# Optimization experiments

Hardware: AMD Instinct MI355X
Metric: run time of the kernel (lower is better)

Reference implementation:

```python
import jax, jax.numpy as jnp
import numpy as np

N_NODES = 100000
N_EDGES = 1600000
IN_FEAT = 64
OUT_FEAT = 64


def setup_inputs() -> dict:
    key = jax.random.key(0)
    k_feat, k_src, k_dst, k_tw, k_tb, k_pw, k_pb = jax.random.split(key, 7)
    bound = 1.0 / np.sqrt(IN_FEAT)
    return {
        "feat": jax.random.normal(k_feat, (N_NODES, IN_FEAT), dtype=jnp.float32),
        "src": jax.random.randint(k_src, (N_EDGES,), 0, N_NODES, dtype=jnp.int32),
        "dst": jax.random.randint(k_dst, (N_EDGES,), 0, N_NODES, dtype=jnp.int32),
        "theta_w": jax.random.uniform(k_tw, (OUT_FEAT, IN_FEAT), jnp.float32, -bound, bound),
        "theta_b": jax.random.uniform(k_tb, (OUT_FEAT,), jnp.float32, -bound, bound),
        "phi_w": jax.random.uniform(k_pw, (OUT_FEAT, IN_FEAT), jnp.float32, -bound, bound),
        "phi_b": jax.random.uniform(k_pb, (OUT_FEAT,), jnp.float32, -bound, bound),
    }


def reference(feat, src, dst, theta_w, theta_b, phi_w, phi_b):
    # Two dense projections: h_theta = theta(feat), h_phi = phi(feat)
    h_theta = feat @ theta_w.T + theta_b          # [N, out_feat]
    h_phi = feat @ phi_w.T + phi_b                # [N, out_feat]
    diff = h_phi - h_theta                        # dstdata['x']
    # u_add_v: per-edge message e = h_theta[src] + (h_phi - h_theta)[dst]
    e = h_theta[src] + diff[dst]                  # [E, out_feat]
    # fn.max('e', 'x'): segment max over destination nodes
    out = jax.ops.segment_max(e, dst, num_segments=N_NODES)  # [N, out_feat]
    # DGL fills zero-in-degree destinations with 0 (segment_max yields -inf)
    return jnp.where(jnp.isfinite(out), out, jnp.float32(0))
```

## Files before the change

### kernel.cpp

```cpp
#include <hip/hip_runtime.h>
#include <hip/hip_bf16.h>
#include <hip/hip_fp16.h>

#define F 64
#define BSH 7
#define NBMAX 1024
#define BPAD 16
#define CHUNK 4096
#define EPT 8
#define BCAP 4096
#define WPAD 72

typedef __bf16 bf16x8 __attribute__((ext_vector_type(8)));
typedef float  f32x4  __attribute__((ext_vector_type(4)));
typedef unsigned int uint4v __attribute__((ext_vector_type(4)));

__device__ inline unsigned pkmax(unsigned a, unsigned b) {
    unsigned d;
    asm volatile("v_pk_max_f16 %0, %1, %2" : "=v"(d) : "v"(a), "v"(b));
    return d;
}
__device__ inline uint4v pkmax4(uint4v a, uint4v b) {
    uint4v r;
    r.x = pkmax(a.x, b.x); r.y = pkmax(a.y, b.y);
    r.z = pkmax(a.z, b.z); r.w = pkmax(a.w, b.w);
    return r;
}
__device__ inline float half_lo(unsigned u) {
    union { unsigned short s; _Float16 h; } c; c.s = (unsigned short)(u & 0xFFFF);
    return (float)c.h;
}
__device__ inline float half_hi(unsigned u) {
    union { unsigned short s; _Float16 h; } c; c.s = (unsigned short)(u >> 16);
    return (float)c.h;
}
__device__ inline void casmax(unsigned* a, unsigned val) {
    unsigned old = *a;
    while (true) {
        unsigned nw = pkmax(old, val);
        if (nw == old) break;
        unsigned prev = atomicCAS(a, old, nw);
        if (prev == old) break;
        old = prev;
    }
}

union FusedSh {
    struct { __bf16 w2t[128 * WPAD]; float bias[128]; } p;
    struct {
        int cur[NBMAX]; int gb[NBMAX]; int lbeg[NBMAX];
        int fs[512];
        unsigned sw[CHUNK];
        unsigned short sb[CHUNK];
    } b;
};

__global__ __launch_bounds__(512) void fused_proj_bin(
    const float* __restrict__ feat,
    const float* __restrict__ theta_w, const float* __restrict__ theta_b,
    const float* __restrict__ phi_w,  const float* __restrict__ phi_b,
    _Float16* __restrict__ h16, _Float16* __restrict__ d16,
    const int* __restrict__ src, const int* __restrict__ dst,
    int* __restrict__ bcnt, unsigned* __restrict__ packed,
    int n_nodes, int n_edges, int nb, int bin_blocks, int proj_blocks)
{
    __shared__ FusedSh sh;
    const int t = threadIdx.x;

    if (blockIdx.x < bin_blocks) {
        const int base = blockIdx.x * CHUNK;
        const int cnt = min(CHUNK, n_edges - base);

        for (int i = t; i < NBMAX; i += 512) sh.b.cur[i] = 0;
        __syncthreads();

        unsigned w[EPT];
        int      bk[EPT];
        int      rk[EPT];
        const int k0 = t * EPT;

        if (k0 + EPT <= cnt) {
            #pragma unroll
            for (int j = 0; j < EPT; ++j) {
                int k = k0 + j;
                int s = src[base + k], d = dst[base + k];
                w[j]  = ((unsigned)(d & ((1 << BSH) - 1)) << 17) | (unsigned)s;
                int b = d >> BSH;
                bk[j] = b;
                rk[j] = atomicAdd(&sh.b.cur[b], 1);
            }
        } else {
            #pragma unroll
            for (int j = 0; j < EPT; ++j) {
                int k = k0 + j;
                bk[j] = -1;
                if (k < cnt) {
                    int s = src[base + k], d = dst[base + k];
                    w[j]  = ((unsigned)(d & ((1 << BSH) - 1)) << 17) | (unsigned)s;
                    int b = d >> BSH;
                    bk[j] = b;
                    rk[j] = atomicAdd(&sh.b.cur[b], 1);
                }
            }
        }
        __syncthreads();

        for (int i = t; i < nb; i += 512) {
            int c = sh.b.cur[i];
            sh.b.gb[i] = c ? atomicAdd(&bcnt[i * BPAD], c) : 0;
        }

        int c0 = sh.b.cur[2 * t];
        int c1 = sh.b.cur[2 * t + 1];
        int s2 = c0 + c1;
        sh.b.fs[t] = s2;
        __syncthreads();
        for (int off = 1; off < 512; off <<= 1) {
            int x = (t >= off) ? sh.b.fs[t - off] : 0;
            __syncthreads();
            sh.b.fs[t] += x;
            __syncthreads();
        }
        {
            int exc = sh.b.fs[t] - s2;
            sh.b.lbeg[2 * t]     = exc;
            sh.b.lbeg[2 * t + 1] = exc + c0;
        }
        __syncthreads();

        #pragma unroll
        for (int j = 0; j < EPT; ++j) {
            if (bk[j] >= 0) {
                int slot = sh.b.lbeg[bk[j]] + rk[j];
                sh.b.sw[slot] = w[j];
                sh.b.sb[slot] = (unsigned short)bk[j];
            }
        }
        __syncthreads();

        #pragma unroll
        for (int r = 0; r < EPT; ++r) {
            int p = r * 512 + t;
            if (p < cnt) {
                int b = sh.b.sb[p];
                int pos = sh.b.gb[b] + (p - sh.b.lbeg[b]);
                if (pos < BCAP) packed[(size_t)b * BCAP + pos] = sh.b.sw[p];
            }
        }
    } else {
        const int pb = blockIdx.x - bin_blocks;

        for (int i = t; i < 128 * 64; i += 512) {
            int n = i >> 6, k = i & 63;
            float v = (n < 64) ? theta_w[n * 64 + k]
                               : phi_w[(n - 64) * 64 + k] - theta_w[(n - 64) * 64 + k];
            sh.p.w2t[n * WPAD + k] = (__bf16)v;
        }
        if (t < 128) {
            int n = t;
            sh.p.bias[n] = (n < 64) ? theta_b[n] : (phi_b[n - 64] - theta_b[n - 64]);
        }
        __syncthreads();

        const int lane = t & 63;
        const int wv   = t >> 6;
        const int m    = lane & 15;
        const int q    = lane >> 4;
        const int nchunks = (n_nodes + 127) >> 7;

        for (int ch = pb; ch < nchunks; ch += proj_blocks) {
            const int rowbase = ch * 128 + wv * 16;
            int arow = rowbase + m;
            int rs = arow < n_nodes ? arow : 0;

            bf16x8 a0, a1;
            {
                const float* p0 = feat + (size_t)rs * 64 + q * 8;
                #pragma unroll
                for (int j = 0; j < 8; ++j) a0[j] = (__bf16)p0[j];
                #pragma unroll
                for (int j = 0; j < 8; ++j) a1[j] = (__bf16)p0[32 + j];
            }

            f32x4 acc[8];
            #pragma unroll
            for (int c = 0; c < 8; ++c) acc[c] = (f32x4){0.f, 0.f, 0.f, 0.f};

            #pragma unroll
            for (int c = 0; c < 8; ++c) {
                const __bf16* wp = &sh.p.w2t[(c * 16 + m) * WPAD + q * 8];
                bf16x8 b0 = *(const bf16x8*)wp;
                bf16x8 b1 = *(const bf16x8*)(wp + 32);
                acc[c] = __builtin_amdgcn_mfma_f32_16x16x32_bf16(a0, b0, acc[c], 0, 0, 0);
                acc[c] = __builtin_amdgcn_mfma_f32_16x16x32_bf16(a1, b1, acc[c], 0, 0, 0);
            }

            #pragma unroll
            for (int c = 0; c < 8; ++c) {
                float bb = sh.p.bias[c * 16 + m];
                #pragma unroll
                for (int r = 0; r < 4; ++r) {
                    int orow = rowbase + q * 4 + r;
                    if (orow < n_nodes) {
                        float v = acc[c][r] + bb;
                        if (c < 4)
                            h16[(size_t)orow * F + c * 16 + m] = (_Float16)v;
                        else
                            d16[(size_t)orow * F + (c - 4) * 16 + m] = (_Float16)v;
                    }
                }
            }
        }
    }
}

__global__ __launch_bounds__(256) void sort_reduce(
    const unsigned* __restrict__ packed, const int* __restrict__ bcnt,
    const _Float16* __restrict__ h16, const _Float16* __restrict__ d16,
    float* __restrict__ out, int n_nodes)
{
    __shared__ unsigned ew[BCAP];
    __shared__ unsigned mx[128 * 32];
    __shared__ int fcnt[128];
    __shared__ int fbg[129];
    __shared__ int fs[256];

    const int b = blockIdx.x, t = threadIdx.x;
    const int beg = b * BCAP;
    const int cnt = min(bcnt[b * BPAD], BCAP);
    const unsigned NEGI = 0xFC00FC00u;

    #pragma unroll
    for (int i = 0; i < 16; ++i) mx[i * 256 + t] = NEGI;
    if (t < 128) fcnt[t] = 0;
    __syncthreads();

    unsigned w[16];
    int      rk[16];
    #pragma unroll
    for (int j = 0; j < 16; ++j) {
        int k = j * 256 + t;
        rk[j] = -1;
        if (k < cnt) {
            unsigned wrd = packed[beg + k];
            w[j]  = wrd;
            rk[j] = atomicAdd(&fcnt[wrd >> 17], 1);
        }
    }
    __syncthreads();

    int v = (t < 128) ? fcnt[t] : 0;
    fs[t] = v;
    __syncthreads();
    for (int off = 1; off < 128; off <<= 1) {
        int x = (t >= off) ? fs[t - off] : 0;
        __syncthreads();
        fs[t] += x;
        __syncthreads();
    }
    if (t < 128) fbg[t] = fs[t] - v;
    if (t == 0)  fbg[128] = cnt;
    __syncthreads();

    #pragma unroll
    for (int j = 0; j < 16; ++j) {
        if (rk[j] >= 0) {
            unsigned wrd = w[j];
            ew[fbg[wrd >> 17] + rk[j]] = wrd & 0x1FFFFu;
        }
    }
    __syncthreads();

    const int g  = t >> 3;
    const int f8 = t & 7;
    {
        int L0 = (cnt + 31) >> 5;
        int L  = ((L0 + 3) & ~7) | 4;
        int s  = g * L; if (s > cnt) s = cnt;
        int e  = s + L; if (e > cnt) e = cnt;

        if (s < e) {
            int lo = 0, hi = 128;
            while (lo + 1 < hi) {
                int mid = (lo + hi) >> 1;
                if (fbg[mid] <= s) lo = mid; else hi = mid;
            }
            int node = lo;
            int nend = fbg[node + 1];

            uint4v acc = (uint4v){NEGI, NEGI, NEGI, NEGI};
            int p = s;
            for (; p + 4 <= e; p += 4) {
                uint4v sv = *(const uint4v*)&ew[p];
                uint4v v0 = *(const uint4v*)(h16 + (size_t)sv.x * F + f8 * 8);
                uint4v v1 = *(const uint4v*)(h16 + (size_t)sv.y * F + f8 * 8);
                uint4v v2 = *(const uint4v*)(h16 + (size_t)sv.z * F + f8 * 8);
                uint4v v3 = *(const uint4v*)(h16 + (size_t)sv.w * F + f8 * 8);
                while (p >= nend) {
                    unsigned* m0 = &mx[node * 32 + f8 * 4];
                    casmax(m0 + 0, acc.x); casmax(m0 + 1, acc.y);
                    casmax(m0 + 2, acc.z); casmax(m0 + 3, acc.w);
                    acc = (uint4v){NEGI, NEGI, NEGI, NEGI};
                    ++node; nend = fbg[node + 1];
                }
                acc = pkmax4(acc, v0);
                while (p + 1 >= nend) {
                    unsigned* m0 = &mx[node * 32 + f8 * 4];
                    casmax(m0 + 0, acc.x); casmax(m0 + 1, acc.y);
                    casmax(m0 + 2, acc.z); casmax(m0 + 3, acc.w);
                    acc = (uint4v){NEGI, NEGI, NEGI, NEGI};
                    ++node; nend = fbg[node + 1];
                }
                acc = pkmax4(acc, v1);
                while (p + 2 >= nend) {
                    unsigned* m0 = &mx[node * 32 + f8 * 4];
                    casmax(m0 + 0, acc.x); casmax(m0 + 1, acc.y);
                    casmax(m0 + 2, acc.z); casmax(m0 + 3, acc.w);
                    acc = (uint4v){NEGI, NEGI, NEGI, NEGI};
                    ++node; nend = fbg[node + 1];
                }
                acc = pkmax4(acc, v2);
                while (p + 3 >= nend) {
                    unsigned* m0 = &mx[node * 32 + f8 * 4];
                    casmax(m0 + 0, acc.x); casmax(m0 + 1, acc.y);
                    casmax(m0 + 2, acc.z); casmax(m0 + 3, acc.w);
                    acc = (uint4v){NEGI, NEGI, NEGI, NEGI};
                    ++node; nend = fbg[node + 1];
                }
                acc = pkmax4(acc, v3);
            }
            for (; p < e; ++p) {
                unsigned srcn = ew[p];
                uint4v v0 = *(const uint4v*)(h16 + (size_t)srcn * F + f8 * 8);
                while (p >= nend) {
                    unsigned* m0 = &mx[node * 32 + f8 * 4];
                    casmax(m0 + 0, acc.x); casmax(m0 + 1, acc.y);
                    casmax(m0 + 2, acc.z); casmax(m0 + 3, acc.w);
                    acc = (uint4v){NEGI, NEGI, NEGI, NEGI};
                    ++node; nend = fbg[node + 1];
                }
                acc = pkmax4(acc, v0);
            }
            unsigned* m0 = &mx[node * 32 + f8 * 4];
            casmax(m0 + 0, acc.x); casmax(m0 + 1, acc.y);
            casmax(m0 + 2, acc.z); casmax(m0 + 3, acc.w);
        }
    }
    __syncthreads();

    const int ln0 = t >> 3;
    #pragma unroll
    for (int pass = 0; pass < 4; ++pass) {
        int ln = ln0 + pass * 32;
        int node = (b << BSH) + ln;
        if (node < n_nodes) {
            size_t o = (size_t)node * F + f8 * 8;
            f32x4 r0, r1;
            if (fcnt[ln] > 0) {
                uint4v A  = *(const uint4v*)&mx[ln * 32 + f8 * 4];
                uint4v dv = __builtin_nontemporal_load((const uint4v*)(d16 + o));
                r0[0] = half_lo(dv.x) + half_lo(A.x);
                r0[1] = half_hi(dv.x) + half_hi(A.x);
                r0[2] = half_lo(dv.y) + half_lo(A.y);
                r0[3] = half_hi(dv.y) + half_hi(A.y);
                r1[0] = half_lo(dv.z) + half_lo(A.z);
                r1[1] = half_hi(dv.z) + half_hi(A.z);
                r1[2] = half_lo(dv.w) + half_lo(A.w);
                r1[3] = half_hi(dv.w) + half_hi(A.w);
            } else {
                r0 = (f32x4){0.f, 0.f, 0.f, 0.f};
                r1 = (f32x4){0.f, 0.f, 0.f, 0.f};
            }
            __builtin_nontemporal_store(r0, (f32x4*)(out + o));
            __builtin_nontemporal_store(r1, (f32x4*)(out + o + 4));
        }
    }
}

extern "C" void kernel_launch(void* const* d_in, const int* in_sizes, int n_in,
                              void* d_out, int out_size, void* d_ws, size_t ws_size,
                              hipStream_t stream) {
    const float* feat    = (const float*)d_in[0];
    const int*   src     = (const int*)d_in[1];
    const int*   dst     = (const int*)d_in[2];
    const float* theta_w = (const float*)d_in[3];
    const float* theta_b = (const float*)d_in[4];
    const float* phi_w   = (const float*)d_in[5];
    const float* phi_b   = (const float*)d_in[6];
    float* out = (float*)d_out;

    const int n_nodes = in_sizes[0] / F;
    const int n_edges = in_sizes[1];
    const int nb      = (n_nodes + (1 << BSH) - 1) >> BSH;

    _Float16* h16    = (_Float16*)d_ws;
    _Float16* d16    = h16 + (size_t)n_nodes * F;
    unsigned* packed = (unsigned*)(d16 + (size_t)n_nodes * F);
    int*      bcnt   = (int*)(packed + (size_t)nb * BCAP);

    hipMemsetAsync(bcnt, 0, NBMAX * BPAD * sizeof(int), stream);

    const int bin_blocks  = (n_edges + CHUNK - 1) / CHUNK;
    const int proj_blocks = 391;
    fused_proj_bin<<<bin_blocks + proj_blocks, 512, 0, stream>>>(
        feat, theta_w, theta_b, phi_w, phi_b, h16, d16,
        src, dst, bcnt, packed, n_nodes, n_edges, nb, bin_blocks, proj_blocks);

    sort_reduce<<<nb, 256, 0, stream>>>(packed, bcnt, h16, d16, out, n_nodes);
}
```

Before: 157.1 us.

## Split fused projection/binning kernel into separate proj and bin kernels

The single launch that ran edge binning and the MFMA projection in different blocks becomes two kernels launched one after the other. The projection kernel now uses one block per 128-row chunk instead of a grid-stride loop over 391 blocks. Each kernel gets its own shared-memory layout instead of sharing a union, so the projection kernel can reach higher occupancy. The cost is an extra launch, and binning and projection no longer run concurrently.

Result: slower. 164.3 us (+4.6%).

```diff
diff --git a/kernel.cpp b/kernel.cpp
--- a/kernel.cpp
+++ b/kernel.cpp
@@ -45,171 +45,167 @@
     }
 }
 
-union FusedSh {
-    struct { __bf16 w2t[128 * WPAD]; float bias[128]; } p;
-    struct {
-        int cur[NBMAX]; int gb[NBMAX]; int lbeg[NBMAX];
-        int fs[512];
-        unsigned sw[CHUNK];
-        unsigned short sb[CHUNK];
-    } b;
-};
-
-__global__ __launch_bounds__(512) void fused_proj_bin(
+
+__global__ __launch_bounds__(512) void proj_kernel(
     const float* __restrict__ feat,
     const float* __restrict__ theta_w, const float* __restrict__ theta_b,
     const float* __restrict__ phi_w,  const float* __restrict__ phi_b,
-    _Float16* __restrict__ h16, _Float16* __restrict__ d16,
+    _Float16* __restrict__ h16, _Float16* __restrict__ d16, int n_nodes)
+{
+    __shared__ __bf16 w2t[128 * WPAD];
+    __shared__ float  bias[128];
+    const int t = threadIdx.x;
+
+    for (int i = t; i < 128 * 64; i += 512) {
+        int n = i >> 6, k = i & 63;
+        float v = (n < 64) ? theta_w[n * 64 + k]
+                           : phi_w[(n - 64) * 64 + k] - theta_w[(n - 64) * 64 + k];
+        w2t[n * WPAD + k] = (__bf16)v;
+    }
+    if (t < 128) {
+        int n = t;
+        bias[n] = (n < 64) ? theta_b[n] : (phi_b[n - 64] - theta_b[n - 64]);
+    }
+    __syncthreads();
+
+    const int lane = t & 63;
+    const int wv   = t >> 6;
+    const int m    = lane & 15;
+    const int q    = lane >> 4;
+
+    const int rowbase = blockIdx.x * 128 + wv * 16;
+    int arow = rowbase + m;
+    int rs = arow < n_nodes ? arow : 0;
+
+    bf16x8 a0, a1;
+    {
+        const float* p0 = feat + (size_t)rs * 64 + q * 8;
+        #pragma unroll
+        for (int j = 0; j < 8; ++j) a0[j] = (__bf16)p0[j];
+        #pragma unroll
+        for (int j = 0; j < 8; ++j) a1[j] = (__bf16)p0[32 + j];
+    }
+
+    f32x4 acc[8];
+    #pragma unroll
+    for (int c = 0; c < 8; ++c) acc[c] = (f32x4){0.f, 0.f, 0.f, 0.f};
+
+    #pragma unroll
+    for (int c = 0; c < 8; ++c) {
+        const __bf16* wp = &w2t[(c * 16 + m) * WPAD + q * 8];
+        bf16x8 b0 = *(const bf16x8*)wp;
+        bf16x8 b1 = *(const bf16x8*)(wp + 32);
+        acc[c] = __builtin_amdgcn_mfma_f32_16x16x32_bf16(a0, b0, acc[c], 0, 0, 0);
+        acc[c] = __builtin_amdgcn_mfma_f32_16x16x32_bf16(a1, b1, acc[c], 0, 0, 0);
+    }
+
+    #pragma unroll
+    for (int c = 0; c < 8; ++c) {
+        float bb = bias[c * 16 + m];
+        #pragma unroll
+        for (int r = 0; r < 4; ++r) {
+            int orow = rowbase + q * 4 + r;
+            if (orow < n_nodes) {
+                float v = acc[c][r] + bb;
+                if (c < 4)
+                    h16[(size_t)orow * F + c * 16 + m] = (_Float16)v;
+                else
+                    d16[(size_t)orow * F + (c - 4) * 16 + m] = (_Float16)v;
+            }
+        }
+    }
+}
+
+__global__ __launch_bounds__(512) void bin_kernel(
     const int* __restrict__ src, const int* __restrict__ dst,
     int* __restrict__ bcnt, unsigned* __restrict__ packed,
-    int n_nodes, int n_edges, int nb, int bin_blocks, int proj_blocks)
+    int n_edges, int nb)
 {
-    __shared__ FusedSh sh;
+    __shared__ int cur[NBMAX];
+    __shared__ int gb[NBMAX];
+    __shared__ int lbeg[NBMAX];
+    __shared__ int fs[512];
+    __shared__ unsigned sw[CHUNK];
+    __shared__ unsigned short sb[CHUNK];
+
     const int t = threadIdx.x;
-
-    if (blockIdx.x < bin_blocks) {
-        const int base = blockIdx.x * CHUNK;
-        const int cnt = min(CHUNK, n_edges - base);
-
-        for (int i = t; i < NBMAX; i += 512) sh.b.cur[i] = 0;
-        __syncthreads();
-
-        unsigned w[EPT];
-        int      bk[EPT];
-        int      rk[EPT];
-        const int k0 = t * EPT;
-
-        if (k0 + EPT <= cnt) {
-            #pragma unroll
-            for (int j = 0; j < EPT; ++j) {
-                int k = k0 + j;
+    const int base = blockIdx.x * CHUNK;
+    const int cnt = min(CHUNK, n_edges - base);
+
+    for (int i = t; i < NBMAX; i += 512) cur[i] = 0;
+    __syncthreads();
+
+    unsigned w[EPT];
+    int      bk[EPT];
+    int      rk[EPT];
+    const int k0 = t * EPT;
+
+    if (k0 + EPT <= cnt) {
+        #pragma unroll
+        for (int j = 0; j < EPT; ++j) {
+            int k = k0 + j;
+            int s = src[base + k], d = dst[base + k];
+            w[j]  = ((unsigned)(d & ((1 << BSH) - 1)) << 17) | (unsigned)s;
+            int b = d >> BSH;
+            bk[j] = b;
+            rk[j] = atomicAdd(&cur[b], 1);
+        }
+    } else {
+        #pragma unroll
+        for (int j = 0; j < EPT; ++j) {
+            int k = k0 + j;
+            bk[j] = -1;
+            if (k < cnt) {
                 int s = src[base + k], d = dst[base + k];
                 w[j]  = ((unsigned)(d & ((1 << BSH) - 1)) << 17) | (unsigned)s;
                 int b = d >> BSH;
                 bk[j] = b;
-                rk[j] = atomicAdd(&sh.b.cur[b], 1);
-            }
-        } else {
-            #pragma unroll
-            for (int j = 0; j < EPT; ++j) {
-                int k = k0 + j;
-                bk[j] = -1;
-                if (k < cnt) {
-                    int s = src[base + k], d = dst[base + k];
-                    w[j]  = ((unsigned)(d & ((1 << BSH) - 1)) << 17) | (unsigned)s;
-                    int b = d >> BSH;
-                    bk[j] = b;
-                    rk[j] = atomicAdd(&sh.b.cur[b], 1);
-                }
-            }
-        }
+                rk[j] = atomicAdd(&cur[b], 1);
+            }
+        }
+    }
+    __syncthreads();
+
+    for (int i = t; i < nb; i += 512) {
+        int c = cur[i];
+        gb[i] = c ? atomicAdd(&bcnt[i * BPAD], c) : 0;
+    }
+
+    int c0 = cur[2 * t];
+    int c1 = cur[2 * t + 1];
+    int s2 = c0 + c1;
+    fs[t] = s2;
+    __syncthreads();
+    for (int off = 1; off < 512; off <<= 1) {
+        int x = (t >= off) ? fs[t - off] : 0;
         __syncthreads();
-
-        for (int i = t; i < nb; i += 512) {
-            int c = sh.b.cur[i];
-            sh.b.gb[i] = c ? atomicAdd(&bcnt[i * BPAD], c) : 0;
-        }
-
-        int c0 = sh.b.cur[2 * t];
-        int c1 = sh.b.cur[2 * t + 1];
-        int s2 = c0 + c1;
-        sh.b.fs[t] = s2;
+        fs[t] += x;
         __syncthreads();
-        for (int off = 1; off < 512; off <<= 1) {
-            int x = (t >= off) ? sh.b.fs[t - off] : 0;
-            __syncthreads();
-            sh.b.fs[t] += x;
-            __syncthreads();
-        }
-        {
-            int exc = sh.b.fs[t] - s2;
-            sh.b.lbeg[2 * t]     = exc;
-            sh.b.lbeg[2 * t + 1] = exc + c0;
-        }
-        __syncthreads();
-
-        #pragma unroll
-        for (int j = 0; j < EPT; ++j) {
-            if (bk[j] >= 0) {
-                int slot = sh.b.lbeg[bk[j]] + rk[j];
-                sh.b.sw[slot] = w[j];
-                sh.b.sb[slot] = (unsigned short)bk[j];
-            }
-        }
-        __syncthreads();
-
-        #pragma unroll
-        for (int r = 0; r < EPT; ++r) {
-            int p = r * 512 + t;
-            if (p < cnt) {
-                int b = sh.b.sb[p];
-                int pos = sh.b.gb[b] + (p - sh.b.lbeg[b]);
-                if (pos < BCAP) packed[(size_t)b * BCAP + pos] = sh.b.sw[p];
-            }
-        }
-    } else {
-        const int pb = blockIdx.x - bin_blocks;
-
-        for (int i = t; i < 128 * 64; i += 512) {
-            int n = i >> 6, k = i & 63;
-            float v = (n < 64) ? theta_w[n * 64 + k]
-                               : phi_w[(n - 64) * 64 + k] - theta_w[(n - 64) * 64 + k];
-            sh.p.w2t[n * WPAD + k] = (__bf16)v;
-        }
-        if (t < 128) {
-            int n = t;
-            sh.p.bias[n] = (n < 64) ? theta_b[n] : (phi_b[n - 64] - theta_b[n - 64]);
-        }
-        __syncthreads();
-
-        const int lane = t & 63;
-        const int wv   = t >> 6;
-        const int m    = lane & 15;
-        const int q    = lane >> 4;
-        const int nchunks = (n_nodes + 127) >> 7;
-
-        for (int ch = pb; ch < nchunks; ch += proj_blocks) {
-            const int rowbase = ch * 128 + wv * 16;
-            int arow = rowbase + m;
-            int rs = arow < n_nodes ? arow : 0;
-
-            bf16x8 a0, a1;
-            {
-                const float* p0 = feat + (size_t)rs * 64 + q * 8;
-                #pragma unroll
-                for (int j = 0; j < 8; ++j) a0[j] = (__bf16)p0[j];
-                #pragma unroll
-                for (int j = 0; j < 8; ++j) a1[j] = (__bf16)p0[32 + j];
-            }
-
-            f32x4 acc[8];
-            #pragma unroll
-            for (int c = 0; c < 8; ++c) acc[c] = (f32x4){0.f, 0.f, 0.f, 0.f};
-
-            #pragma unroll
-            for (int c = 0; c < 8; ++c) {
-                const __bf16* wp = &sh.p.w2t[(c * 16 + m) * WPAD + q * 8];
-                bf16x8 b0 = *(const bf16x8*)wp;
-                bf16x8 b1 = *(const bf16x8*)(wp + 32);
-                acc[c] = __builtin_amdgcn_mfma_f32_16x16x32_bf16(a0, b0, acc[c], 0, 0, 0);
-                acc[c] = __builtin_amdgcn_mfma_f32_16x16x32_bf16(a1, b1, acc[c], 0, 0, 0);
-            }
-
-            #pragma unroll
-            for (int c = 0; c < 8; ++c) {
-                float bb = sh.p.bias[c * 16 + m];
-                #pragma unroll
-                for (int r = 0; r < 4; ++r) {
-                    int orow = rowbase + q * 4 + r;
-                    if (orow < n_nodes) {
-                        float v = acc[c][r] + bb;
-                        if (c < 4)
-                            h16[(size_t)orow * F + c * 16 + m] = (_Float16)v;
-                        else
-                            d16[(size_t)orow * F + (c - 4) * 16 + m] = (_Float16)v;
-                    }
-                }
-            }
+    }
+    {
+        int exc = fs[t] - s2;
+        lbeg[2 * t]     = exc;
+        lbeg[2 * t + 1] = exc + c0;
+    }
+    __syncthreads();
+
+    #pragma unroll
+    for (int j = 0; j < EPT; ++j) {
+        if (bk[j] >= 0) {
+            int slot = lbeg[bk[j]] + rk[j];
+            sw[slot] = w[j];
+            sb[slot] = (unsigned short)bk[j];
+        }
+    }
+    __syncthreads();
+
+    #pragma unroll
+    for (int r = 0; r < EPT; ++r) {
+        int p = r * 512 + t;
+        if (p < cnt) {
+            int b = sb[p];
+            int pos = gb[b] + (p - lbeg[b]);
+            if (pos < BCAP) packed[(size_t)b * BCAP + pos] = sw[p];
         }
     }
 }
@@ -400,11 +396,13 @@
 
     hipMemsetAsync(bcnt, 0, NBMAX * BPAD * sizeof(int), stream);
 
-    const int bin_blocks  = (n_edges + CHUNK - 1) / CHUNK;
-    const int proj_blocks = 391;
-    fused_proj_bin<<<bin_blocks + proj_blocks, 512, 0, stream>>>(
-        feat, theta_w, theta_b, phi_w, phi_b, h16, d16,
-        src, dst, bcnt, packed, n_nodes, n_edges, nb, bin_blocks, proj_blocks);
+    const int proj_blocks = (n_nodes + 127) / 128;
+    proj_kernel<<<proj_blocks, 512, 0, stream>>>(
+        feat, theta_w, theta_b, phi_w, phi_b, h16, d16, n_nodes);
+
+    const int bin_blocks = (n_edges + CHUNK - 1) / CHUNK;
+    bin_kernel<<<bin_blocks, 512, 0, stream>>>(src, dst, bcnt, packed,
+                                               n_edges, nb);
 
     sort_reduce<<<nb, 256, 0, stream>>>(packed, bcnt, h16, d16, out, n_nodes);
 }
```
